# Performance work log

Measured on AMD Instinct MI355X. Metric: run time of the kernel, lower is better.

Reference implementation:

```python
import jax, jax.numpy as jnp
import numpy as np


def setup_inputs() -> dict:
    key = jax.random.key(0)
    ks = jax.random.split(key, 9)
    N, L, E, H = 8, 4096, 1024, 16
    D = E // H
    return {
        "values": jax.random.normal(ks[0], (N, L, E), dtype=jnp.float32),
        "keys": jax.random.normal(ks[1], (N, L, E), dtype=jnp.float32),
        "query": jax.random.normal(ks[2], (N, L, E), dtype=jnp.float32),
        "mask": jax.random.randint(ks[3], (1, 1, H, H), 0, 2, dtype=jnp.int32),
        "Wv": jax.random.normal(ks[4], (D, D), dtype=jnp.float32) / np.sqrt(D),
        "Wk": jax.random.normal(ks[5], (D, D), dtype=jnp.float32) / np.sqrt(D),
        "Wq": jax.random.normal(ks[6], (D, D), dtype=jnp.float32) / np.sqrt(D),
        "Wo": jax.random.normal(ks[7], (E, E), dtype=jnp.float32) / np.sqrt(E),
        "bo": jnp.zeros((E,), dtype=jnp.float32),
    }


def reference(values, keys, query, mask, Wv, Wk, Wq, Wo, bo):
    N, L, E = query.shape
    H = mask.shape[-1]          # heads
    D = E // H                  # head_dim
    # reshape to (N, L, H, D) then per-head Dense(head_dim) on last dim
    v = values.reshape(N, L, H, D) @ Wv
    k = keys.reshape(N, L, H, D) @ Wk
    q = query.reshape(N, L, H, D) @ Wq
    # Faithful to the source: keys transposed with perm [0,1,3,2], so matmul
    # batches over (N, L) and energy is a (H x H) matrix per position.
    energy = jnp.einsum("nlhd,nlgd->nlhg", q, k)  # (N, L, H, H)
    energy = jnp.where(mask == 0, jnp.float32(-1e20), energy)
    attention = jax.nn.softmax(energy / (E ** 0.5), axis=-1)
    out = jnp.einsum("nlhg,nlgd->nlhd", attention, v)  # (N, L, H, D)
    # source: transpose to (N, H, L, D) then reshape to (N, L, H*D)
    out = out.transpose(0, 2, 1, 3).reshape(N, L, H * D)
    out = out @ Wo + bo
    return out, attention
```

## Files before the change

### kernel.cpp

```cpp
#include <hip/hip_runtime.h>

typedef short short8 __attribute__((ext_vector_type(8)));
typedef short short4v __attribute__((ext_vector_type(4)));
typedef float f32x4 __attribute__((ext_vector_type(4)));
typedef unsigned short u16;

#define MFMA16(a, b, c) __builtin_amdgcn_mfma_f32_16x16x32_bf16(a, b, c, 0, 0, 0)
#define GLD_LDS(g, l)                                                          \
  __builtin_amdgcn_global_load_lds(                                            \
      (__attribute__((address_space(1))) void*)(void*)(g),                     \
      (__attribute__((address_space(3))) void*)(l), 16, 0, 0)

__device__ __forceinline__ u16 f2bf(float f) {
  union { float f; unsigned u; } x; x.f = f;
  unsigned r = x.u + 0x7fffu + ((x.u >> 16) & 1u);
  return (u16)(r >> 16);
}

__device__ __forceinline__ short4v pack4(f32x4 a) {
  short4v r;
  r[0] = (short)f2bf(a[0]); r[1] = (short)f2bf(a[1]);
  r[2] = (short)f2bf(a[2]); r[3] = (short)f2bf(a[3]);
  return r;
}

__global__ __launch_bounds__(256) void prep(const float* __restrict__ Wv,
                                            const float* __restrict__ Wk,
                                            const float* __restrict__ Wq,
                                            const float* __restrict__ Wo,
                                            u16* __restrict__ WoT2,
                                            u16* __restrict__ Mt) {
  __shared__ __align__(16) float A[64][65];
  __shared__ __align__(16) float B[64][68];
  const int t = threadIdx.x;
  const int r = t >> 2, c = (t & 3) * 16;
  if (blockIdx.x < 256) {
    const int tr = blockIdx.x >> 4, tc = blockIdx.x & 15;
#pragma unroll
    for (int u = 0; u < 4; ++u)
      *(float4*)&A[r][c + u * 4] = *(const float4*)(Wv + r * 64 + c + u * 4);
#pragma unroll
    for (int u = 0; u < 4; ++u)
      *(float4*)&B[r][c + u * 4] =
          *(const float4*)(Wo + (tr * 64 + r) * 1024 + tc * 64 + c + u * 4);
    __syncthreads();
    const int n = t & 63, i0 = (t >> 6) * 16;
    float acc[16];
#pragma unroll
    for (int ii = 0; ii < 16; ++ii) acc[ii] = 0.f;
    for (int j = 0; j < 64; ++j) {
      const float wo = B[j][n];
#pragma unroll
      for (int ii = 0; ii < 16; ++ii) acc[ii] += A[i0 + ii][j] * wo;
    }
    u16* dst = WoT2 + (size_t)(tc * 64 + n) * 1024 + tr * 64 + i0;
    short8 o0, o1;
#pragma unroll
    for (int jj = 0; jj < 8; ++jj) { o0[jj] = (short)f2bf(acc[jj]); o1[jj] = (short)f2bf(acc[8 + jj]); }
    *(short8*)(void*)dst = o0;
    *(short8*)(void*)(dst + 8) = o1;
  } else {
#pragma unroll
    for (int u = 0; u < 4; ++u)
      *(float4*)&A[r][c + u * 4] = *(const float4*)(Wq + r * 64 + c + u * 4);
#pragma unroll
    for (int u = 0; u < 4; ++u)
      *(float4*)&B[r][c + u * 4] = *(const float4*)(Wk + r * 64 + c + u * 4);
    __syncthreads();
    const int n = t & 63, k0 = (t >> 6) * 16;
    float acc[16];
#pragma unroll
    for (int ii = 0; ii < 16; ++ii) acc[ii] = 0.f;
    for (int d = 0; d < 64; ++d) {
      const float wk = B[n][d];
#pragma unroll
      for (int kk = 0; kk < 16; ++kk) acc[kk] += A[k0 + kk][d] * wk;
    }
    u16* dst = Mt + n * 64 + k0;
    short8 o0, o1;
#pragma unroll
    for (int jj = 0; jj < 8; ++jj) { o0[jj] = (short)f2bf(acc[jj]); o1[jj] = (short)f2bf(acc[8 + jj]); }
    *(short8*)(void*)dst = o0;
    *(short8*)(void*)(dst + 8) = o1;
  }
}

__global__ __launch_bounds__(256, 4) void attn_kernel(
    const float* __restrict__ values, const float* __restrict__ keys,
    const float* __restrict__ query, const int* __restrict__ mask,
    const u16* __restrict__ Mt, float* __restrict__ attn,
    u16* __restrict__ out2) {
  __shared__ __align__(16) u16 x1[4][16][68];
  __shared__ __align__(16) u16 x2[4][16][68];
  __shared__ __align__(16) u16 vT[4][64][24];
  __shared__ __align__(16) u16 mt_lds[64][68];
  __shared__ int mask_lds[256];

  const int tid = threadIdx.x;
  const int w = tid >> 6, lane = tid & 63;
  const int g16 = lane & 15;
  const int q4 = lane >> 4;
  const int kbase = q4 * 8;
  const int mrow = q4 * 4;

  {
    const short8* mg = (const short8*)Mt;
    short8 a0 = mg[tid];
    short8 a1 = mg[256 + tid];
    *(short8*)&mt_lds[tid >> 3][(tid & 7) * 8] = a0;
    const int g1 = 256 + tid;
    *(short8*)&mt_lds[g1 >> 3][(g1 & 7) * 8] = a1;
    mask_lds[tid] = mask[tid];
  }
  __syncthreads();

  int mzb = 0;
#pragma unroll
  for (int r = 0; r < 4; ++r)
    mzb |= (mask_lds[(mrow + r) * 16 + g16] == 0) ? (1 << r) : 0;

  const f32x4 zero = {0.f, 0.f, 0.f, 0.f};
  const int p = blockIdx.x * 4 + w;

  const f32x4* qv = (const f32x4*)(query + (size_t)p * 1024);
  const f32x4* kv = (const f32x4*)(keys + (size_t)p * 1024);
  const f32x4* vv = (const f32x4*)(values + (size_t)p * 1024);
  f32x4 qf0 = qv[lane], qf1 = qv[64 + lane], qf2 = qv[128 + lane], qf3 = qv[192 + lane];
  f32x4 kf0 = kv[lane], kf1 = kv[64 + lane], kf2 = kv[128 + lane], kf3 = kv[192 + lane];
  f32x4 vf0 = vv[lane], vf1 = vv[64 + lane], vf2 = vv[128 + lane], vf3 = vv[192 + lane];

  const int wr = lane >> 4;
  const int wc = (lane & 15) * 4;
  *(short4v*)&x1[w][0 + wr][wc] = pack4(qf0);
  *(short4v*)&x1[w][4 + wr][wc] = pack4(qf1);
  *(short4v*)&x1[w][8 + wr][wc] = pack4(qf2);
  *(short4v*)&x1[w][12 + wr][wc] = pack4(qf3);
  *(short4v*)&x2[w][0 + wr][wc] = pack4(kf0);
  *(short4v*)&x2[w][4 + wr][wc] = pack4(kf1);
  *(short4v*)&x2[w][8 + wr][wc] = pack4(kf2);
  *(short4v*)&x2[w][12 + wr][wc] = pack4(kf3);
#pragma unroll
  for (int i = 0; i < 4; ++i) {
    vT[w][wc + i][0 + wr] = f2bf(vf0[i]);
    vT[w][wc + i][4 + wr] = f2bf(vf1[i]);
    vT[w][wc + i][8 + wr] = f2bf(vf2[i]);
    vT[w][wc + i][12 + wr] = f2bf(vf3[i]);
  }

  short8 aq0 = *(const short8*)&x1[w][g16][kbase];
  short8 aq1 = *(const short8*)&x1[w][g16][32 + kbase];
  short8 ak0 = *(const short8*)&x2[w][g16][kbase];
  short8 ak1 = *(const short8*)&x2[w][g16][32 + kbase];
  short8 mtf[2][4];
#pragma unroll
  for (int kb = 0; kb < 2; ++kb)
#pragma unroll
    for (int nc = 0; nc < 4; ++nc)
      mtf[kb][nc] = *(const short8*)&mt_lds[nc * 16 + g16][kb * 32 + kbase];

  f32x4 tacc[4];
#pragma unroll
  for (int nc = 0; nc < 4; ++nc) {
    tacc[nc] = MFMA16(aq0, mtf[0][nc], zero);
    tacc[nc] = MFMA16(aq1, mtf[1][nc], tacc[nc]);
  }
#pragma unroll
  for (int nc = 0; nc < 4; ++nc)
#pragma unroll
    for (int r = 0; r < 4; ++r)
      x1[w][mrow + r][nc * 16 + g16] = f2bf(tacc[nc][r]);

  short8 ea0 = *(const short8*)&x1[w][g16][kbase];
  short8 ea1 = *(const short8*)&x1[w][g16][32 + kbase];
  f32x4 acce = MFMA16(ea0, ak0, zero);
  acce = MFMA16(ea1, ak1, acce);

  const float SC = 0.045084220027780106f;
  float* x1f = (float*)&x1[w][0][0];
#pragma unroll
  for (int r = 0; r < 4; ++r) {
    const float val = ((mzb >> r) & 1) ? -45.f : acce[r] * SC;
    const float pe = exp2f(val);
    float s = pe;
    s += __shfl_xor(s, 1, 16);
    s += __shfl_xor(s, 2, 16);
    s += __shfl_xor(s, 4, 16);
    s += __shfl_xor(s, 8, 16);
    const float a = pe * __builtin_amdgcn_rcpf(s);
    x1f[(mrow + r) * 34 + g16] = a;
    x2[w][mrow + r][g16] = f2bf(a);
  }

  {
    f32x4 av = *(const f32x4*)&x1f[(lane >> 2) * 34 + (lane & 3) * 4];
    *(f32x4*)(attn + (size_t)p * 256 + lane * 4) = av;
  }

  short8 pa;
  if (lane < 32) {
    pa = *(const short8*)&x2[w][g16][kbase];
  } else {
    short8 z = {0, 0, 0, 0, 0, 0, 0, 0};
    pa = z;
  }
  const int gsel = (lane < 32) ? kbase : 0;
#pragma unroll
  for (int nc = 0; nc < 4; ++nc) {
    short8 vb = *(const short8*)&vT[w][nc * 16 + g16][gsel];
    f32x4 acco = MFMA16(pa, vb, zero);
#pragma unroll
    for (int r = 0; r < 4; ++r)
      x1[w][mrow + r][nc * 16 + g16] = f2bf(acco[r]);
  }

  {
    short8 s0 = *(const short8*)&x1[w][lane >> 3][(lane & 7) * 8];
    short8 s1 = *(const short8*)&x1[w][8 + (lane >> 3)][(lane & 7) * 8];
    u16* dst = out2 + (size_t)p * 1024 + lane * 8;
    *(short8*)(void*)dst = s0;
    *(short8*)(void*)(dst + 512) = s1;
  }
}

__global__ __launch_bounds__(256, 2) void gemm_kernel(
    const u16* __restrict__ A, const u16* __restrict__ BT,
    const float* __restrict__ bo, float* __restrict__ C) {
  __shared__ __align__(16) u16 As[128 * 32];
  __shared__ __align__(16) u16 Bs[128 * 32];
  const int t = threadIdx.x, lane = t & 63;
  const int g16 = lane & 15, q4 = lane >> 4;
  const int w = t >> 6, wm = w >> 1, wn = w & 1;
  const int bm = blockIdx.x & 255, bn = blockIdx.x >> 8;

  f32x4 acc[4][4];
  const f32x4 zero = {0.f, 0.f, 0.f, 0.f};
#pragma unroll
  for (int mt = 0; mt < 4; ++mt)
#pragma unroll
    for (int nt = 0; nt < 4; ++nt) acc[mt][nt] = zero;

  const int am = t >> 2, ak = (t & 3) * 8;
  const int R0 = bm * 128 + am;
  const int R1 = R0 + 64;
  const size_t base0 =
      ((size_t)((R0 >> 12) * 4096 + (R0 & 255) * 16)) * 1024 +
      ((R0 & 4095) >> 8) * 64;
  const size_t base1 =
      ((size_t)((R1 >> 12) * 4096 + (R1 & 255) * 16)) * 1024 +
      ((R1 & 4095) >> 8) * 64;
  const u16* ga0 = A + base0 + ak;
  const u16* ga1 = A + base1 + ak;
  const u16* gb = BT + (size_t)(bn * 128 + am) * 1024 + ak;
  u16* lA = &As[t * 8];
  u16* lB = &Bs[t * 8];

  for (int kt = 0; kt < 32; ++kt) {
    __syncthreads();
    const int aoff = (kt >> 1) * 1024 + (kt & 1) * 32;
    const int ko = kt * 32;
    GLD_LDS(ga0 + aoff, lA);
    GLD_LDS(ga1 + aoff, lA + 2048);
    GLD_LDS(gb + ko, lB);
    GLD_LDS(gb + 64 * 1024 + ko, lB + 2048);
    __syncthreads();

    short8 af[4], bf[4];
#pragma unroll
    for (int mt = 0; mt < 4; ++mt)
      af[mt] = *(const short8*)&As[(wm * 64 + mt * 16 + g16) * 32 + q4 * 8];
#pragma unroll
    for (int nt = 0; nt < 4; ++nt)
      bf[nt] = *(const short8*)&Bs[(wn * 64 + nt * 16 + g16) * 32 + q4 * 8];
#pragma unroll
    for (int mt = 0; mt < 4; ++mt)
#pragma unroll
      for (int nt = 0; nt < 4; ++nt)
        acc[mt][nt] = MFMA16(af[mt], bf[nt], acc[mt][nt]);
  }

#pragma unroll
  for (int nt = 0; nt < 4; ++nt) {
    const int col = bn * 128 + wn * 64 + nt * 16 + g16;
    const float bias = bo[col];
#pragma unroll
    for (int mt = 0; mt < 4; ++mt) {
#pragma unroll
      for (int r = 0; r < 4; ++r) {
        const int row = bm * 128 + wm * 64 + mt * 16 + q4 * 4 + r;
        C[(size_t)row * 1024 + col] = acc[mt][nt][r] + bias;
      }
    }
  }
}

extern "C" void kernel_launch(void* const* d_in, const int* in_sizes, int n_in,
                              void* d_out, int out_size, void* d_ws,
                              size_t ws_size, hipStream_t stream) {
  const float* values = (const float*)d_in[0];
  const float* keys   = (const float*)d_in[1];
  const float* query  = (const float*)d_in[2];
  const int*   mask   = (const int*)d_in[3];
  const float* Wv = (const float*)d_in[4];
  const float* Wk = (const float*)d_in[5];
  const float* Wq = (const float*)d_in[6];
  const float* Wo = (const float*)d_in[7];
  const float* bo = (const float*)d_in[8];

  float* out  = (float*)d_out;
  float* attn = out + 33554432;

  u16* out2 = (u16*)d_ws;
  u16* WoT2 = out2 + 33554432;
  u16* Mt   = WoT2 + 1048576;

  prep<<<257, 256, 0, stream>>>(Wv, Wk, Wq, Wo, WoT2, Mt);
  attn_kernel<<<8192, 256, 0, stream>>>(values, keys, query, mask, Mt, attn,
                                        out2);
  gemm_kernel<<<2048, 256, 0, stream>>>(out2, WoT2, bo, out);
}
```

Measured before the change: 233.7 us.

## Process four positions per wave with register prefetch of next inputs

Each attention block now handles 16 positions instead of 4, so each wave loops over four positions and the grid shrinks to a quarter of its former size. The per-block setup (mask and Mt staging into LDS) is amortized over more work. Inside the loop, the q/k/v loads for the next position are issued right after the current position's data is written to LDS, so global load latency overlaps with MFMA and softmax work. The cost is higher register pressure from holding prefetched data and fewer blocks available to hide latency.

```diff
diff --git a/kernel.cpp b/kernel.cpp
--- a/kernel.cpp
+++ b/kernel.cpp
@@ -120,105 +120,120 @@
     mzb |= (mask_lds[(mrow + r) * 16 + g16] == 0) ? (1 << r) : 0;
 
   const f32x4 zero = {0.f, 0.f, 0.f, 0.f};
-  const int p = blockIdx.x * 4 + w;
-
-  const f32x4* qv = (const f32x4*)(query + (size_t)p * 1024);
-  const f32x4* kv = (const f32x4*)(keys + (size_t)p * 1024);
-  const f32x4* vv = (const f32x4*)(values + (size_t)p * 1024);
-  f32x4 qf0 = qv[lane], qf1 = qv[64 + lane], qf2 = qv[128 + lane], qf3 = qv[192 + lane];
-  f32x4 kf0 = kv[lane], kf1 = kv[64 + lane], kf2 = kv[128 + lane], kf3 = kv[192 + lane];
-  f32x4 vf0 = vv[lane], vf1 = vv[64 + lane], vf2 = vv[128 + lane], vf3 = vv[192 + lane];
+  const int pbase = blockIdx.x * 16 + w * 4;
+
+  const f32x4* qv = (const f32x4*)query;
+  const f32x4* kv = (const f32x4*)keys;
+  const f32x4* vv = (const f32x4*)values;
+  const size_t b0 = (size_t)pbase * 256 + lane;
+
+  f32x4 qf0 = qv[b0], qf1 = qv[b0 + 64], qf2 = qv[b0 + 128], qf3 = qv[b0 + 192];
+  f32x4 kf0 = kv[b0], kf1 = kv[b0 + 64], kf2 = kv[b0 + 128], kf3 = kv[b0 + 192];
+  f32x4 vf0 = vv[b0], vf1 = vv[b0 + 64], vf2 = vv[b0 + 128], vf3 = vv[b0 + 192];
 
   const int wr = lane >> 4;
   const int wc = (lane & 15) * 4;
-  *(short4v*)&x1[w][0 + wr][wc] = pack4(qf0);
-  *(short4v*)&x1[w][4 + wr][wc] = pack4(qf1);
-  *(short4v*)&x1[w][8 + wr][wc] = pack4(qf2);
-  *(short4v*)&x1[w][12 + wr][wc] = pack4(qf3);
-  *(short4v*)&x2[w][0 + wr][wc] = pack4(kf0);
-  *(short4v*)&x2[w][4 + wr][wc] = pack4(kf1);
-  *(short4v*)&x2[w][8 + wr][wc] = pack4(kf2);
-  *(short4v*)&x2[w][12 + wr][wc] = pack4(kf3);
+
 #pragma unroll
   for (int i = 0; i < 4; ++i) {
-    vT[w][wc + i][0 + wr] = f2bf(vf0[i]);
-    vT[w][wc + i][4 + wr] = f2bf(vf1[i]);
-    vT[w][wc + i][8 + wr] = f2bf(vf2[i]);
-    vT[w][wc + i][12 + wr] = f2bf(vf3[i]);
-  }
-
-  short8 aq0 = *(const short8*)&x1[w][g16][kbase];
-  short8 aq1 = *(const short8*)&x1[w][g16][32 + kbase];
-  short8 ak0 = *(const short8*)&x2[w][g16][kbase];
-  short8 ak1 = *(const short8*)&x2[w][g16][32 + kbase];
-  short8 mtf[2][4];
-#pragma unroll
-  for (int kb = 0; kb < 2; ++kb)
+    const int p = pbase + i;
+
+    *(short4v*)&x1[w][0 + wr][wc] = pack4(qf0);
+    *(short4v*)&x1[w][4 + wr][wc] = pack4(qf1);
+    *(short4v*)&x1[w][8 + wr][wc] = pack4(qf2);
+    *(short4v*)&x1[w][12 + wr][wc] = pack4(qf3);
+    *(short4v*)&x2[w][0 + wr][wc] = pack4(kf0);
+    *(short4v*)&x2[w][4 + wr][wc] = pack4(kf1);
+    *(short4v*)&x2[w][8 + wr][wc] = pack4(kf2);
+    *(short4v*)&x2[w][12 + wr][wc] = pack4(kf3);
+#pragma unroll
+    for (int j = 0; j < 4; ++j) {
+      vT[w][wc + j][0 + wr] = f2bf(vf0[j]);
+      vT[w][wc + j][4 + wr] = f2bf(vf1[j]);
+      vT[w][wc + j][8 + wr] = f2bf(vf2[j]);
+      vT[w][wc + j][12 + wr] = f2bf(vf3[j]);
+    }
+
+    if (i < 3) {
+      const size_t nb = b0 + (size_t)(i + 1) * 256;
+      qf0 = qv[nb]; qf1 = qv[nb + 64]; qf2 = qv[nb + 128]; qf3 = qv[nb + 192];
+      kf0 = kv[nb]; kf1 = kv[nb + 64]; kf2 = kv[nb + 128]; kf3 = kv[nb + 192];
+      vf0 = vv[nb]; vf1 = vv[nb + 64]; vf2 = vv[nb + 128]; vf3 = vv[nb + 192];
+    }
+
+    short8 aq0 = *(const short8*)&x1[w][g16][kbase];
+    short8 aq1 = *(const short8*)&x1[w][g16][32 + kbase];
+    short8 ak0 = *(const short8*)&x2[w][g16][kbase];
+    short8 ak1 = *(const short8*)&x2[w][g16][32 + kbase];
+    short8 mtf[2][4];
+#pragma unroll
+    for (int kb = 0; kb < 2; ++kb)
+#pragma unroll
+      for (int nc = 0; nc < 4; ++nc)
+        mtf[kb][nc] = *(const short8*)&mt_lds[nc * 16 + g16][kb * 32 + kbase];
+
+    f32x4 tacc[4];
+#pragma unroll
+    for (int nc = 0; nc < 4; ++nc) {
+      tacc[nc] = MFMA16(aq0, mtf[0][nc], zero);
+      tacc[nc] = MFMA16(aq1, mtf[1][nc], tacc[nc]);
+    }
 #pragma unroll
     for (int nc = 0; nc < 4; ++nc)
-      mtf[kb][nc] = *(const short8*)&mt_lds[nc * 16 + g16][kb * 32 + kbase];
-
-  f32x4 tacc[4];
-#pragma unroll
-  for (int nc = 0; nc < 4; ++nc) {
-    tacc[nc] = MFMA16(aq0, mtf[0][nc], zero);
-    tacc[nc] = MFMA16(aq1, mtf[1][nc], tacc[nc]);
-  }
-#pragma unroll
-  for (int nc = 0; nc < 4; ++nc)
-#pragma unroll
-    for (int r = 0; r < 4; ++r)
-      x1[w][mrow + r][nc * 16 + g16] = f2bf(tacc[nc][r]);
-
-  short8 ea0 = *(const short8*)&x1[w][g16][kbase];
-  short8 ea1 = *(const short8*)&x1[w][g16][32 + kbase];
-  f32x4 acce = MFMA16(ea0, ak0, zero);
-  acce = MFMA16(ea1, ak1, acce);
-
-  const float SC = 0.045084220027780106f;
-  float* x1f = (float*)&x1[w][0][0];
-#pragma unroll
-  for (int r = 0; r < 4; ++r) {
-    const float val = ((mzb >> r) & 1) ? -45.f : acce[r] * SC;
-    const float pe = exp2f(val);
-    float s = pe;
-    s += __shfl_xor(s, 1, 16);
-    s += __shfl_xor(s, 2, 16);
-    s += __shfl_xor(s, 4, 16);
-    s += __shfl_xor(s, 8, 16);
-    const float a = pe * __builtin_amdgcn_rcpf(s);
-    x1f[(mrow + r) * 34 + g16] = a;
-    x2[w][mrow + r][g16] = f2bf(a);
-  }
-
-  {
-    f32x4 av = *(const f32x4*)&x1f[(lane >> 2) * 34 + (lane & 3) * 4];
-    *(f32x4*)(attn + (size_t)p * 256 + lane * 4) = av;
-  }
-
-  short8 pa;
-  if (lane < 32) {
-    pa = *(const short8*)&x2[w][g16][kbase];
-  } else {
-    short8 z = {0, 0, 0, 0, 0, 0, 0, 0};
-    pa = z;
-  }
-  const int gsel = (lane < 32) ? kbase : 0;
-#pragma unroll
-  for (int nc = 0; nc < 4; ++nc) {
-    short8 vb = *(const short8*)&vT[w][nc * 16 + g16][gsel];
-    f32x4 acco = MFMA16(pa, vb, zero);
-#pragma unroll
-    for (int r = 0; r < 4; ++r)
-      x1[w][mrow + r][nc * 16 + g16] = f2bf(acco[r]);
-  }
-
-  {
-    short8 s0 = *(const short8*)&x1[w][lane >> 3][(lane & 7) * 8];
-    short8 s1 = *(const short8*)&x1[w][8 + (lane >> 3)][(lane & 7) * 8];
-    u16* dst = out2 + (size_t)p * 1024 + lane * 8;
-    *(short8*)(void*)dst = s0;
-    *(short8*)(void*)(dst + 512) = s1;
+#pragma unroll
+      for (int r = 0; r < 4; ++r)
+        x1[w][mrow + r][nc * 16 + g16] = f2bf(tacc[nc][r]);
+
+    short8 ea0 = *(const short8*)&x1[w][g16][kbase];
+    short8 ea1 = *(const short8*)&x1[w][g16][32 + kbase];
+    f32x4 acce = MFMA16(ea0, ak0, zero);
+    acce = MFMA16(ea1, ak1, acce);
+
+    const float SC = 0.045084220027780106f;
+    float* x1f = (float*)&x1[w][0][0];
+#pragma unroll
+    for (int r = 0; r < 4; ++r) {
+      const float val = ((mzb >> r) & 1) ? -45.f : acce[r] * SC;
+      const float pe = exp2f(val);
+      float s = pe;
+      s += __shfl_xor(s, 1, 16);
+      s += __shfl_xor(s, 2, 16);
+      s += __shfl_xor(s, 4, 16);
+      s += __shfl_xor(s, 8, 16);
+      const float a = pe * __builtin_amdgcn_rcpf(s);
+      x1f[(mrow + r) * 34 + g16] = a;
+      x2[w][mrow + r][g16] = f2bf(a);
+    }
+
+    {
+      f32x4 av = *(const f32x4*)&x1f[(lane >> 2) * 34 + (lane & 3) * 4];
+      *(f32x4*)(attn + (size_t)p * 256 + lane * 4) = av;
+    }
+
+    short8 pa;
+    if (lane < 32) {
+      pa = *(const short8*)&x2[w][g16][kbase];
+    } else {
+      short8 z = {0, 0, 0, 0, 0, 0, 0, 0};
+      pa = z;
+    }
+    const int gsel = (lane < 32) ? kbase : 0;
+#pragma unroll
+    for (int nc = 0; nc < 4; ++nc) {
+      short8 vb = *(const short8*)&vT[w][nc * 16 + g16][gsel];
+      f32x4 acco = MFMA16(pa, vb, zero);
+#pragma unroll
+      for (int r = 0; r < 4; ++r)
+        x1[w][mrow + r][nc * 16 + g16] = f2bf(acco[r]);
+    }
+
+    {
+      short8 s0 = *(const short8*)&x1[w][lane >> 3][(lane & 7) * 8];
+      short8 s1 = *(const short8*)&x1[w][8 + (lane >> 3)][(lane & 7) * 8];
+      u16* dst = out2 + (size_t)p * 1024 + lane * 8;
+      *(short8*)(void*)dst = s0;
+      *(short8*)(void*)(dst + 512) = s1;
+    }
   }
 }
 
@@ -314,7 +329,7 @@
   u16* Mt   = WoT2 + 1048576;
 
   prep<<<257, 256, 0, stream>>>(Wv, Wk, Wq, Wo, WoT2, Mt);
-  attn_kernel<<<8192, 256, 0, stream>>>(values, keys, query, mask, Mt, attn,
+  attn_kernel<<<2048, 256, 0, stream>>>(values, keys, query, mask, Mt, attn,
                                         out2);
   gemm_kernel<<<2048, 256, 0, stream>>>(out2, WoT2, bo, out);
 }
```

Result: no change. 234.6 us (+0.4%).
